# Optimization experiments

Hardware: AMD Instinct MI355X
Metric: run time of the kernel (lower is better)

## Reference

```python
import jax, jax.numpy as jnp
import numpy as np

B, N, E = 4, 2048, 512
H = 8
HD = E // H
HIDDEN = 3 * E  # split_ratio=3
EPS = 1e-5


def _layernorm(x, g, b):
    mu = jnp.mean(x, axis=-1, keepdims=True)
    var = jnp.var(x, axis=-1, keepdims=True)
    return (x - mu) * jax.lax.rsqrt(var + EPS) * g + b


def setup_inputs() -> dict:
    key = jax.random.key(0)
    ks = jax.random.split(key, 7)
    s = 0.02
    return {
        "x": jax.random.normal(ks[0], (B, N, E), jnp.float32),
        "qkv_w": jax.random.normal(ks[1], (E, 3 * E), jnp.float32) * s,
        "qkv_b": jax.random.normal(ks[2], (3 * E,), jnp.float32) * s,
        "fc1_w": jax.random.normal(ks[3], (E, HIDDEN), jnp.float32) * s,
        "fc1_b": jax.random.normal(ks[4], (HIDDEN,), jnp.float32) * s,
        "fc2_w": jax.random.normal(ks[5], (HIDDEN, E), jnp.float32) * s,
        "fc2_b": jax.random.normal(ks[6], (E,), jnp.float32) * s,
        "ln_att_g": jnp.ones((E,), jnp.float32),
        "ln_att_b": jnp.zeros((E,), jnp.float32),
        "ln_ffn_g": jnp.ones((E,), jnp.float32),
        "ln_ffn_b": jnp.zeros((E,), jnp.float32),
    }


def reference(x, qkv_w, qkv_b, fc1_w, fc1_b, fc2_w, fc2_b,
              ln_att_g, ln_att_b, ln_ffn_g, ln_ffn_b):
    # --- attention sub-block (pre-norm) ---
    h = x
    xn = _layernorm(x, ln_att_g, ln_att_b)
    qkv = xn @ qkv_w + qkv_b                     # [B,N,3E]
    qkv = qkv.reshape(B, N, H, 3 * HD).transpose(0, 2, 1, 3)  # [B,H,N,3*HD]
    q, k, v = jnp.split(qkv, 3, axis=-1)         # each [B,H,N,HD]
    scale = HD ** -0.5
    scores = jnp.einsum("bhnd,bhmd->bhnm", q, k) * scale
    attn = jax.nn.softmax(scores, axis=-1)
    out = jnp.einsum("bhnm,bhmd->bhnd", attn, v)
    out = out.transpose(0, 2, 1, 3).reshape(B, N, E)
    x = out + h
    # --- FFN sub-block (pre-norm) ---
    h = x
    xn = _layernorm(x, ln_ffn_g, ln_ffn_b)
    y = jax.nn.gelu(xn @ fc1_w + fc1_b, approximate=False)
    y = y @ fc2_w + fc2_b
    return y + h
```

## Files before the change

### kernel.cpp

```cpp
#include <hip/hip_runtime.h>
#include <hip/hip_bf16.h>
#include <math.h>

typedef unsigned short ushort_t;
typedef unsigned int   uint32;

typedef __bf16 bf16x8 __attribute__((ext_vector_type(8)));
typedef float  floatx4 __attribute__((ext_vector_type(4)));

__device__ __forceinline__ float lo16(uint32 u) { return __uint_as_float(u << 16); }
__device__ __forceinline__ float hi16(uint32 u) { return __uint_as_float(u & 0xFFFF0000u); }
__device__ __forceinline__ float b2f(ushort_t u) { return __uint_as_float(((uint32)u) << 16); }
__device__ __forceinline__ ushort_t f2b(float f) {
    uint32 x = __float_as_uint(f);
    x += 0x7FFFu + ((x >> 16) & 1u);
    return (ushort_t)(x >> 16);
}
__device__ __forceinline__ bool bf_mode(const uint32* sniff) {
    return *sniff == 0x3F803F80u;
}
__device__ __forceinline__ float rd(const void* p, size_t i, bool bf) {
    return bf ? b2f(((const ushort_t*)p)[i]) : ((const float*)p)[i];
}
__device__ __forceinline__ float4 rd4(const void* p, size_t i, bool bf) {
    if (bf) {
        uint2 u = *(const uint2*)((const ushort_t*)p + i);
        float4 r; r.x = lo16(u.x); r.y = hi16(u.x); r.z = lo16(u.y); r.w = hi16(u.y);
        return r;
    }
    return *(const float4*)((const float*)p + i);
}
__device__ __forceinline__ float fexp2(float x) {
#if __has_builtin(__builtin_amdgcn_exp2f)
    return __builtin_amdgcn_exp2f(x);
#else
    return exp2f(x);
#endif
}
__device__ __forceinline__ uint32 pack_bf16(float e0, float e1) {
#if __has_builtin(__builtin_amdgcn_perm)
    return __builtin_amdgcn_perm(__float_as_uint(e1), __float_as_uint(e0), 0x07060302u);
#else
    return (__float_as_uint(e0) >> 16) | (__float_as_uint(e1) & 0xFFFF0000u);
#endif
}
__device__ __forceinline__ void async_cp16(const ushort_t* g, ushort_t* l) {
    __builtin_amdgcn_global_load_lds(
        (const __attribute__((address_space(1))) void*)g,
        (__attribute__((address_space(3))) void*)l, 16, 0, 0);
}
__device__ __forceinline__ float gelu_f(float x) {
    float u = 0.79788456f * x * (1.0f + 0.044715f * x * x);
    u = fminf(u, 40.0f);
    float e = exp2f(u * 2.88539008f);
    return x * e * __builtin_amdgcn_rcpf(e + 1.0f);
}

__global__ __launch_bounds__(256)
void sentinel(float* out, float val, int n)
{
    int i = blockIdx.x * 256 + threadIdx.x;
    if (i < n) out[i] = val;
}

__global__ __launch_bounds__(256)
void conv_transpose3(const void* __restrict__ w0, const void* __restrict__ w1,
                     const void* __restrict__ w2, ushort_t* __restrict__ t0,
                     ushort_t* __restrict__ t1, ushort_t* __restrict__ t2,
                     const uint32* __restrict__ sniff)
{
    __shared__ ushort_t s[32][33];
    bool bf = bf_mode(sniff);
    int z = blockIdx.y;
    const void* W  = (z == 0) ? w0 : (z == 1) ? w1 : w2;
    ushort_t* Wt   = (z == 0) ? t0 : (z == 1) ? t1 : t2;
    int K = (z == 2) ? 1536 : 512;
    int N = (z == 2) ? 512 : 1536;
    int nb = N >> 5;
    int bx = blockIdx.x;
    int n0 = (bx % nb) * 32, k0 = (bx / nb) * 32;

    int tx = threadIdx.x & 31, ty = threadIdx.x >> 5;
#pragma unroll
    for (int i = 0; i < 4; i++) {
        int r = ty + i * 8;
        size_t idx = (size_t)(k0 + r) * N + (n0 + tx);
        s[r][tx] = f2b(rd(W, idx, bf));
    }
    __syncthreads();
#pragma unroll
    for (int i = 0; i < 4; i++) {
        int r = ty + i * 8;
        Wt[(size_t)(n0 + r) * K + (k0 + tx)] = s[tx][r];
    }
}

__global__ __launch_bounds__(256)
void v_transpose(const ushort_t* __restrict__ hbuf, ushort_t* __restrict__ vt)
{
    __shared__ ushort_t s[32][33];
    int tx = threadIdx.x & 31, ty = threadIdx.x >> 5;
    int n0 = blockIdx.x * 32, d0 = blockIdx.y * 32;
    int bh = blockIdx.z;
    int b = bh >> 3, h = bh & 7;
#pragma unroll
    for (int i = 0; i < 4; i++) {
        int r = ty + i * 8;
        s[r][tx] = hbuf[(size_t)(b * 2048 + n0 + r) * 1536 + h * 192 + 128 + d0 + tx];
    }
    __syncthreads();
#pragma unroll
    for (int i = 0; i < 4; i++) {
        int r = ty + i * 8;
        vt[((size_t)bh * 64 + d0 + r) * 2048 + n0 + tx] = s[tx][r];
    }
}

template <int XMODE>
__global__ __launch_bounds__(256)
void ln_any(const void* __restrict__ x, const void* __restrict__ g,
            const void* __restrict__ bta, ushort_t* __restrict__ out,
            const uint32* __restrict__ sniff)
{
    bool bf = bf_mode(sniff);
    int wid = threadIdx.x >> 6, lane = threadIdx.x & 63;
    int row = blockIdx.x * 4 + wid;
    size_t base = (size_t)row * 512 + (size_t)lane * 8;

    float4 v0, v1;
    if (XMODE == 2) { v0 = rd4(x, base, false); v1 = rd4(x, base + 4, false); }
    else            { v0 = rd4(x, base, bf);    v1 = rd4(x, base + 4, bf); }
    float v[8] = {v0.x, v0.y, v0.z, v0.w, v1.x, v1.y, v1.z, v1.w};

    float s = 0.f, ss = 0.f;
#pragma unroll
    for (int i = 0; i < 8; i++) { s += v[i]; ss += v[i] * v[i]; }
#pragma unroll
    for (int off = 32; off; off >>= 1) {
        s  += __shfl_xor(s, off);
        ss += __shfl_xor(ss, off);
    }
    float mu  = s * (1.0f / 512.0f);
    float var = ss * (1.0f / 512.0f) - mu * mu;
    float rs  = rsqrtf(var + 1e-5f);

    float4 g0 = rd4(g, lane * 8, bf), g1 = rd4(g, lane * 8 + 4, bf);
    float4 b0 = rd4(bta, lane * 8, bf), b1 = rd4(bta, lane * 8 + 4, bf);
    float gv[8] = {g0.x, g0.y, g0.z, g0.w, g1.x, g1.y, g1.z, g1.w};
    float bv[8] = {b0.x, b0.y, b0.z, b0.w, b1.x, b1.y, b1.z, b1.w};

    ushort_t o[8];
#pragma unroll
    for (int i = 0; i < 8; i++) o[i] = f2b((v[i] - mu) * rs * gv[i] + bv[i]);
    uint4 ov;
    ov.x = (uint32)o[0] | ((uint32)o[1] << 16);
    ov.y = (uint32)o[2] | ((uint32)o[3] << 16);
    ov.z = (uint32)o[4] | ((uint32)o[5] << 16);
    ov.w = (uint32)o[6] | ((uint32)o[7] << 16);
    *(uint4*)(out + base) = ov;
}

template <int TJ, int MODE>
__global__ __launch_bounds__(256)
void gemm_bt(const ushort_t* __restrict__ A, const ushort_t* __restrict__ Bt,
             const void* __restrict__ bias, void* C,
             const float* resid, int M, int N, int K,
             const uint32* __restrict__ sniff)
{
    constexpr int BN = 32 * TJ;
    __shared__ ushort_t As[128][32];
    __shared__ ushort_t Bs[BN][32];

    bool bf = bf_mode(sniff);
    int tid = threadIdx.x;
    int wid = tid >> 6, lane = tid & 63;

    int nwgx = gridDim.x;
    int wg   = blockIdx.y * nwgx + blockIdx.x;
    int cpx  = (nwgx * gridDim.y) >> 3;
    int swz  = (wg & 7) * cpx + (wg >> 3);
    int m0 = (swz / nwgx) * 128, n0 = (swz % nwgx) * BN;

    int wm = (wid >> 1) * 64, wn = (wid & 1) * (16 * TJ);
    int lm = lane & 15, kq = lane >> 4;

    floatx4 acc[4][TJ];
#pragma unroll
    for (int i = 0; i < 4; i++)
#pragma unroll
        for (int j = 0; j < TJ; j++) acc[i][j] = (floatx4)(0.f);

    for (int k0 = 0; k0 < K; k0 += 32) {
        __syncthreads();
#pragma unroll
        for (int i = 0; i < 2; i++) {
            int lin = i * 256 + tid;
            int r = lin >> 2, c8 = (lin & 3) * 8;
            async_cp16(&A[(size_t)(m0 + r) * K + k0 + c8], &As[r][c8]);
        }
#pragma unroll
        for (int i = 0; i < BN / 64; i++) {
            int lin = i * 256 + tid;
            int r = lin >> 2, c8 = (lin & 3) * 8;
            async_cp16(&Bt[(size_t)(n0 + r) * K + k0 + c8], &Bs[r][c8]);
        }
        __syncthreads();

        bf16x8 af[4], bfr[TJ];
#pragma unroll
        for (int ti = 0; ti < 4; ti++)
            af[ti] = *(const bf16x8*)&As[wm + ti * 16 + lm][kq * 8];
#pragma unroll
        for (int tj = 0; tj < TJ; tj++)
            bfr[tj] = *(const bf16x8*)&Bs[wn + tj * 16 + lm][kq * 8];
#pragma unroll
        for (int ti = 0; ti < 4; ti++)
#pragma unroll
            for (int tj = 0; tj < TJ; tj++)
                acc[ti][tj] = __builtin_amdgcn_mfma_f32_16x16x32_bf16(
                    af[ti], bfr[tj], acc[ti][tj], 0, 0, 0);
    }

    float bv[TJ];
#pragma unroll
    for (int tj = 0; tj < TJ; tj++) bv[tj] = rd(bias, n0 + wn + tj * 16 + lm, bf);
#pragma unroll
    for (int ti = 0; ti < 4; ti++) {
        int grow_base = m0 + wm + ti * 16 + kq * 4;
#pragma unroll
        for (int tj = 0; tj < TJ; tj++) {
            int gcol = n0 + wn + tj * 16 + lm;
#pragma unroll
            for (int r = 0; r < 4; r++) {
                int grow = grow_base + r;
                float v = acc[ti][tj][r] + bv[tj];
                if (MODE == 1) v = gelu_f(v);
                if (MODE == 2) {
                    float rv = resid[(size_t)grow * N + gcol];
                    ((float*)C)[(size_t)grow * N + gcol] = v + rv;
                } else {
                    ((ushort_t*)C)[(size_t)grow * N + gcol] = f2b(v);
                }
            }
        }
    }
}

template <int MODE>
__global__ __launch_bounds__(256)
void vgemm(const ushort_t* __restrict__ A, const void* __restrict__ W,
           const void* __restrict__ bias, void* C,
           const float* resid, int M, int N, int K,
             const uint32* __restrict__ sniff)
{
    __shared__ float Ast[32][33];
    __shared__ float Bs[32][36];

    bool bf = bf_mode(sniff);
    int t  = threadIdx.x;
    int tx = t & 15, ty = t >> 4;
    int m0 = blockIdx.y * 32, n0 = blockIdx.x * 32;
    int sr = t >> 3, sc4 = (t & 7) * 4;

    float a00 = 0.f, a01 = 0.f, a10 = 0.f, a11 = 0.f;

    for (int k0 = 0; k0 < K; k0 += 32) {
        __syncthreads();
        {
            uint2 u = *(const uint2*)&A[(size_t)(m0 + sr) * K + k0 + sc4];
            Ast[sc4 + 0][sr] = lo16(u.x);
            Ast[sc4 + 1][sr] = hi16(u.x);
            Ast[sc4 + 2][sr] = lo16(u.y);
            Ast[sc4 + 3][sr] = hi16(u.y);
        }
        {
            float4 w = rd4(W, (size_t)(k0 + sr) * N + n0 + sc4, bf);
            *(float4*)&Bs[sr][sc4] = w;
        }
        __syncthreads();

#pragma unroll
        for (int kk = 0; kk < 32; kk++) {
            float av0 = Ast[kk][ty], av1 = Ast[kk][ty + 16];
            float bv0 = Bs[kk][tx],  bv1 = Bs[kk][tx + 16];
            a00 += av0 * bv0; a01 += av0 * bv1;
            a10 += av1 * bv0; a11 += av1 * bv1;
        }
    }

    float accs[4] = {a00, a01, a10, a11};
#pragma unroll
    for (int q = 0; q < 4; q++) {
        int row = m0 + ty + (q >> 1) * 16;
        int col = n0 + tx + (q & 1) * 16;
        float v = accs[q] + rd(bias, col, bf);
        if (MODE == 1) v = gelu_f(v);
        if (MODE == 2) {
            float rv = resid[(size_t)row * N + col];
            ((float*)C)[(size_t)row * N + col] = v + rv;
        } else {
            ((ushort_t*)C)[(size_t)row * N + col] = f2b(v);
        }
    }
}

__global__ __launch_bounds__(256)
void attn_flash(const ushort_t* __restrict__ qkv, const ushort_t* __restrict__ vt,
                const void* __restrict__ x, float* __restrict__ out,
                const uint32* __restrict__ sniff)
{
    __shared__ ushort_t Kl[2][64][72];
    __shared__ ushort_t Vl[2][64][72];

    bool bf = bf_mode(sniff);
    int tid = threadIdx.x;
    int wid = tid >> 6, lane = tid & 63;
    int lm = lane & 15, quad = lane >> 4;

    int bid = blockIdx.x;
    int swz = (bid & 7) * 64 + (bid >> 3);
    int qt = swz & 15;
    int h  = (swz >> 4) & 7;
    int b  = swz >> 7;
    int bh = b * 8 + h;
    int q0 = qt * 128;

    const float SC = 0.18033688011f;

    bf16x8 qf[2][2];
#pragma unroll
    for (int g = 0; g < 2; g++) {
        const ushort_t* qp = qkv +
            ((size_t)(b * 2048 + q0 + wid * 32 + g * 16 + lm) * 1536 + h * 192);
        union { bf16x8 v; ushort_t u[8]; } qa0, qa1;
        qa0.v = *(const bf16x8*)(qp + quad * 8);
        qa1.v = *(const bf16x8*)(qp + 32 + quad * 8);
#pragma unroll
        for (int i = 0; i < 8; i++) {
            qa0.u[i] = f2b(b2f(qa0.u[i]) * SC);
            qa1.u[i] = f2b(b2f(qa1.u[i]) * SC);
        }
        qf[g][0] = qa0.v; qf[g][1] = qa1.v;
    }

    floatx4 oacc[2][4];
#pragma unroll
    for (int g = 0; g < 2; g++)
#pragma unroll
        for (int dt = 0; dt < 4; dt++) oacc[g][dt] = (floatx4)(0.f);
    float lsum[2] = {0.f, 0.f};

    int srow = tid >> 3;
    int sc8  = (tid & 7) * 8;

    const ushort_t* kb0 = qkv + ((size_t)(b * 2048 + srow)      * 1536 + h * 192 + 64 + sc8);
    const ushort_t* kb1 = qkv + ((size_t)(b * 2048 + 32 + srow) * 1536 + h * 192 + 64 + sc8);
    const ushort_t* vb0 = vt + ((size_t)bh * 64 + srow)      * 2048 + sc8;
    const ushort_t* vb1 = vt + ((size_t)bh * 64 + 32 + srow) * 2048 + sc8;

    uint4 kr0 = *(const uint4*)(kb0);
    uint4 kr1 = *(const uint4*)(kb1);
    uint4 vr0 = *(const uint4*)(vb0);
    uint4 vr1 = *(const uint4*)(vb1);
    *(uint4*)&Kl[0][srow][sc8]      = kr0;
    *(uint4*)&Kl[0][32 + srow][sc8] = kr1;
    *(uint4*)&Vl[0][srow][sc8]      = vr0;
    *(uint4*)&Vl[0][32 + srow][sc8] = vr1;
    kr0 = *(const uint4*)(kb0 + (size_t)64 * 1536);
    kr1 = *(const uint4*)(kb1 + (size_t)64 * 1536);
    vr0 = *(const uint4*)(vb0 + 64);
    vr1 = *(const uint4*)(vb1 + 64);
    __syncthreads();

    int addr0 = (lm + ((quad & 1) << 5)) << 2;
    int addr1 = addr0 + 64;
    bool hiq  = (quad >> 1) != 0;

    int p = 0;
    for (int kv = 0; kv < 2048; kv += 64) {
        if (kv < 2048 - 64) {
            *(uint4*)&Kl[p ^ 1][srow][sc8]      = kr0;
            *(uint4*)&Kl[p ^ 1][32 + srow][sc8] = kr1;
            *(uint4*)&Vl[p ^ 1][srow][sc8]      = vr0;
            *(uint4*)&Vl[p ^ 1][32 + srow][sc8] = vr1;
            int nkv = (kv + 128) & 2047;
            kr0 = *(const uint4*)(kb0 + (size_t)nkv * 1536);
            kr1 = *(const uint4*)(kb1 + (size_t)nkv * 1536);
            vr0 = *(const uint4*)(vb0 + nkv);
            vr1 = *(const uint4*)(vb1 + nkv);
        }

        floatx4 sacc[2][4];
#pragma unroll
        for (int g = 0; g < 2; g++)
#pragma unroll
            for (int t = 0; t < 4; t++) sacc[g][t] = (floatx4)(0.f);
        __builtin_amdgcn_s_setprio(1);
#pragma unroll
        for (int t = 0; t < 4; t++) {
            bf16x8 kf0 = *(const bf16x8*)&Kl[p][t * 16 + lm][quad * 8];
            bf16x8 kf1 = *(const bf16x8*)&Kl[p][t * 16 + lm][32 + quad * 8];
#pragma unroll
            for (int g = 0; g < 2; g++) {
                sacc[g][t] = __builtin_amdgcn_mfma_f32_16x16x32_bf16(kf0, qf[g][0], sacc[g][t], 0, 0, 0);
                sacc[g][t] = __builtin_amdgcn_mfma_f32_16x16x32_bf16(kf1, qf[g][1], sacc[g][t], 0, 0, 0);
            }
        }
        __builtin_amdgcn_s_setprio(0);

        uint32 pk[2][4][2];
#pragma unroll
        for (int g = 0; g < 2; g++) {
#pragma unroll
            for (int t = 0; t < 4; t++) {
                float e0 = fexp2(sacc[g][t][0]);
                float e1 = fexp2(sacc[g][t][1]);
                float e2 = fexp2(sacc[g][t][2]);
                float e3 = fexp2(sacc[g][t][3]);
                lsum[g] += (e0 + e1) + (e2 + e3);
                pk[g][t][0] = pack_bf16(e0, e1);
                pk[g][t][1] = pack_bf16(e2, e3);
            }
        }

        bf16x8 pf[2][2];
#pragma unroll
        for (int g = 0; g < 2; g++) {
#pragma unroll
            for (int c = 0; c < 2; c++) {
                uint32 pw[4];
#pragma unroll
                for (int j = 0; j < 4; j++) {
                    int ad = (j >> 1) ? addr1 : addr0;
                    int va = __builtin_amdgcn_ds_bpermute(ad, (int)pk[g][2 * c][j & 1]);
                    int vb = __builtin_amdgcn_ds_bpermute(ad, (int)pk[g][2 * c + 1][j & 1]);
                    pw[j] = (uint32)(hiq ? vb : va);
                }
                union { uint4 u; bf16x8 v; } cv;
                cv.u = make_uint4(pw[0], pw[1], pw[2], pw[3]);
                pf[g][c] = cv.v;
            }
        }

        __builtin_amdgcn_s_setprio(1);
#pragma unroll
        for (int dt = 0; dt < 4; dt++) {
            bf16x8 vf0 = *(const bf16x8*)&Vl[p][dt * 16 + lm][quad * 8];
            bf16x8 vf1 = *(const bf16x8*)&Vl[p][dt * 16 + lm][32 + quad * 8];
#pragma unroll
            for (int g = 0; g < 2; g++) {
                oacc[g][dt] = __builtin_amdgcn_mfma_f32_16x16x32_bf16(pf[g][0], vf0, oacc[g][dt], 0, 0, 0);
                oacc[g][dt] = __builtin_amdgcn_mfma_f32_16x16x32_bf16(pf[g][1], vf1, oacc[g][dt], 0, 0, 0);
            }
        }
        __builtin_amdgcn_s_setprio(0);

        __syncthreads();
        p ^= 1;
    }

    float rinv[2][4];
#pragma unroll
    for (int g = 0; g < 2; g++) {
        float rs = lsum[g];
        rs += __shfl_xor(rs, 16);
        rs += __shfl_xor(rs, 32);
        float ri = __builtin_amdgcn_rcpf(rs);
#pragma unroll
        for (int r = 0; r < 4; r++)
            rinv[g][r] = __shfl(ri, quad * 4 + r);
    }

#pragma unroll
    for (int g = 0; g < 2; g++)
#pragma unroll
        for (int dt = 0; dt < 4; dt++) {
#pragma unroll
            for (int r = 0; r < 4; r++) {
                int row = q0 + wid * 32 + g * 16 + quad * 4 + r;
                int col = h * 64 + dt * 16 + lm;
                size_t idx = (size_t)(b * 2048 + row) * 512 + col;
                out[idx] = oacc[g][dt][r] * rinv[g][r] + rd(x, idx, bf);
            }
        }
}

extern "C" void kernel_launch(void* const* d_in, const int* in_sizes, int n_in,
                              void* d_out, int out_size, void* d_ws, size_t ws_size,
                              hipStream_t stream)
{
    static const int expect[11] = {4194304, 786432, 1536, 786432, 1536, 786432,
                                   512, 512, 512, 512, 512};
    bool ok = (n_in == 11);
    if (ok) for (int i = 0; i < 11; i++) if (in_sizes[i] != expect[i]) { ok = false; break; }
    int nblk = (out_size + 255) / 256;
    if (!ok) {
        sentinel<<<nblk, 256, 0, stream>>>((float*)d_out, 1.0e6f, out_size);
        return;
    }
    if (ws_size < (size_t)33554432) {
        sentinel<<<nblk, 256, 0, stream>>>((float*)d_out, 2.0e6f, out_size);
        return;
    }

    const void* x     = d_in[0];
    const void* qkv_w = d_in[1];
    const void* qkv_b = d_in[2];
    const void* fc1_w = d_in[3];
    const void* fc1_b = d_in[4];
    const void* fc2_w = d_in[5];
    const void* fc2_b = d_in[6];
    const void* ln1g  = d_in[7];
    const void* ln1b  = d_in[8];
    const void* ln2g  = d_in[9];
    const void* ln2b  = d_in[10];
    const uint32* sniff = (const uint32*)d_in[7];

    char* ws = (char*)d_ws;
    ushort_t* xn   = (ushort_t*)(ws);
    ushort_t* hbuf = (ushort_t*)(ws + 8388608);
    float*    x2   = (float*)d_out;
    ushort_t* vt   = xn;

    bool mfma_path = (ws_size >= (size_t)38273024);

    if (mfma_path) {
        ushort_t* wtq = (ushort_t*)(ws + 33554432);
        ushort_t* wt1 = (ushort_t*)(ws + 35127296);
        ushort_t* wt2 = (ushort_t*)(ws + 36700160);

        conv_transpose3<<<dim3(768, 3), 256, 0, stream>>>(qkv_w, fc1_w, fc2_w,
                                                          wtq, wt1, wt2, sniff);
        ln_any<0><<<2048, 256, 0, stream>>>(x, ln1g, ln1b, xn, sniff);
        gemm_bt<4, 0><<<dim3(12, 64), 256, 0, stream>>>(xn, wtq, qkv_b, hbuf, nullptr,
                                                        8192, 1536, 512, sniff);
        v_transpose<<<dim3(64, 2, 32), 256, 0, stream>>>(hbuf, vt);
        attn_flash<<<512, 256, 0, stream>>>(hbuf, vt, x, x2, sniff);
        ln_any<2><<<2048, 256, 0, stream>>>(x2, ln2g, ln2b, xn, sniff);
        gemm_bt<4, 1><<<dim3(12, 64), 256, 0, stream>>>(xn, wt1, fc1_b, hbuf, nullptr,
                                                        8192, 1536, 512, sniff);
        gemm_bt<2, 2><<<dim3(8, 64), 256, 0, stream>>>(hbuf, wt2, fc2_b, d_out, x2,
                                                       8192, 512, 1536, sniff);
    } else {
        ln_any<0><<<2048, 256, 0, stream>>>(x, ln1g, ln1b, xn, sniff);
        vgemm<0><<<dim3(48, 256), 256, 0, stream>>>(xn, qkv_w, qkv_b, hbuf, nullptr,
                                                    8192, 1536, 512, sniff);
        v_transpose<<<dim3(64, 2, 32), 256, 0, stream>>>(hbuf, vt);
        attn_flash<<<512, 256, 0, stream>>>(hbuf, vt, x, x2, sniff);
        ln_any<2><<<2048, 256, 0, stream>>>(x2, ln2g, ln2b, xn, sniff);
        vgemm<1><<<dim3(48, 256), 256, 0, stream>>>(xn, fc1_w, fc1_b, hbuf, nullptr,
                                                    8192, 1536, 512, sniff);
        vgemm<2><<<dim3(16, 256), 256, 0, stream>>>(hbuf, fc2_w, fc2_b, d_out, x2,
                                                    8192, 512, 1536, sniff);
    }
}
```

Measured before the change: 260.6 us.

## Load K/V fragments directly from global into registers in single-wave attention blocks

The flash-attention kernel now runs one 64-thread wave per block, with 2048 blocks each covering 32 query rows. It drops the shared-memory K/V double buffer and its barriers. K fragments are software-pipelined in registers (prefetching the next tile while computing scores), and V fragments are loaded straight from global memory each iteration. This removes LDS traffic and __syncthreads, but K/V are no longer shared across four waves, so global/L2 read traffic rises about fourfold and latency is hidden only by register prefetch and occupancy.

```diff
diff --git a/kernel.cpp b/kernel.cpp
--- a/kernel.cpp
+++ b/kernel.cpp
@@ -304,26 +304,22 @@
     }
 }
 
-__global__ __launch_bounds__(256)
+__global__ __launch_bounds__(64)
 void attn_flash(const ushort_t* __restrict__ qkv, const ushort_t* __restrict__ vt,
                 const void* __restrict__ x, float* __restrict__ out,
                 const uint32* __restrict__ sniff)
 {
-    __shared__ ushort_t Kl[2][64][72];
-    __shared__ ushort_t Vl[2][64][72];
-
     bool bf = bf_mode(sniff);
-    int tid = threadIdx.x;
-    int wid = tid >> 6, lane = tid & 63;
+    int lane = threadIdx.x & 63;
     int lm = lane & 15, quad = lane >> 4;
 
     int bid = blockIdx.x;
-    int swz = (bid & 7) * 64 + (bid >> 3);
-    int qt = swz & 15;
-    int h  = (swz >> 4) & 7;
-    int b  = swz >> 7;
+    int swz = (bid & 7) * 256 + (bid >> 3);
+    int qt = swz & 63;
+    int h  = (swz >> 6) & 7;
+    int b  = swz >> 9;
     int bh = b * 8 + h;
-    int q0 = qt * 128;
+    int q0 = qt * 32;
 
     const float SC = 0.18033688011f;
 
@@ -331,7 +327,7 @@
 #pragma unroll
     for (int g = 0; g < 2; g++) {
         const ushort_t* qp = qkv +
-            ((size_t)(b * 2048 + q0 + wid * 32 + g * 16 + lm) * 1536 + h * 192);
+            ((size_t)(b * 2048 + q0 + g * 16 + lm) * 1536 + h * 192);
         union { bf16x8 v; ushort_t u[8]; } qa0, qa1;
         qa0.v = *(const bf16x8*)(qp + quad * 8);
         qa1.v = *(const bf16x8*)(qp + 32 + quad * 8);
@@ -350,45 +346,27 @@
         for (int dt = 0; dt < 4; dt++) oacc[g][dt] = (floatx4)(0.f);
     float lsum[2] = {0.f, 0.f};
 
-    int srow = tid >> 3;
-    int sc8  = (tid & 7) * 8;
-
-    const ushort_t* kb0 = qkv + ((size_t)(b * 2048 + srow)      * 1536 + h * 192 + 64 + sc8);
-    const ushort_t* kb1 = qkv + ((size_t)(b * 2048 + 32 + srow) * 1536 + h * 192 + 64 + sc8);
-    const ushort_t* vb0 = vt + ((size_t)bh * 64 + srow)      * 2048 + sc8;
-    const ushort_t* vb1 = vt + ((size_t)bh * 64 + 32 + srow) * 2048 + sc8;
-
-    uint4 kr0 = *(const uint4*)(kb0);
-    uint4 kr1 = *(const uint4*)(kb1);
-    uint4 vr0 = *(const uint4*)(vb0);
-    uint4 vr1 = *(const uint4*)(vb1);
-    *(uint4*)&Kl[0][srow][sc8]      = kr0;
-    *(uint4*)&Kl[0][32 + srow][sc8] = kr1;
-    *(uint4*)&Vl[0][srow][sc8]      = vr0;
-    *(uint4*)&Vl[0][32 + srow][sc8] = vr1;
-    kr0 = *(const uint4*)(kb0 + (size_t)64 * 1536);
-    kr1 = *(const uint4*)(kb1 + (size_t)64 * 1536);
-    vr0 = *(const uint4*)(vb0 + 64);
-    vr1 = *(const uint4*)(vb1 + 64);
-    __syncthreads();
+    const ushort_t* kfp = qkv + ((size_t)(b * 2048 + lm) * 1536 + h * 192 + 64 + quad * 8);
+    const ushort_t* vfp = vt + ((size_t)(bh * 64 + lm) * 2048 + quad * 8);
 
     int addr0 = (lm + ((quad & 1) << 5)) << 2;
     int addr1 = addr0 + 64;
     bool hiq  = (quad >> 1) != 0;
 
-    int p = 0;
-    for (int kv = 0; kv < 2048; kv += 64) {
-        if (kv < 2048 - 64) {
-            *(uint4*)&Kl[p ^ 1][srow][sc8]      = kr0;
-            *(uint4*)&Kl[p ^ 1][32 + srow][sc8] = kr1;
-            *(uint4*)&Vl[p ^ 1][srow][sc8]      = vr0;
-            *(uint4*)&Vl[p ^ 1][32 + srow][sc8] = vr1;
-            int nkv = (kv + 128) & 2047;
-            kr0 = *(const uint4*)(kb0 + (size_t)nkv * 1536);
-            kr1 = *(const uint4*)(kb1 + (size_t)nkv * 1536);
-            vr0 = *(const uint4*)(vb0 + nkv);
-            vr1 = *(const uint4*)(vb1 + nkv);
-        }
+    bf16x8 kfA[4][2], kfB[4][2];
+#pragma unroll
+    for (int t = 0; t < 4; t++)
+#pragma unroll
+        for (int c = 0; c < 2; c++)
+            kfA[t][c] = *(const bf16x8*)(kfp + (size_t)(t * 16) * 1536 + c * 32);
+
+    auto iter = [&](int kv, bf16x8 (&kfU)[4][2], bf16x8 (&kfP)[4][2], int nkv) {
+        bf16x8 vf[4][2];
+#pragma unroll
+        for (int dt = 0; dt < 4; dt++)
+#pragma unroll
+            for (int c = 0; c < 2; c++)
+                vf[dt][c] = *(const bf16x8*)(vfp + (size_t)(dt * 16) * 2048 + kv + c * 32);
 
         floatx4 sacc[2][4];
 #pragma unroll
@@ -398,15 +376,19 @@
         __builtin_amdgcn_s_setprio(1);
 #pragma unroll
         for (int t = 0; t < 4; t++) {
-            bf16x8 kf0 = *(const bf16x8*)&Kl[p][t * 16 + lm][quad * 8];
-            bf16x8 kf1 = *(const bf16x8*)&Kl[p][t * 16 + lm][32 + quad * 8];
 #pragma unroll
             for (int g = 0; g < 2; g++) {
-                sacc[g][t] = __builtin_amdgcn_mfma_f32_16x16x32_bf16(kf0, qf[g][0], sacc[g][t], 0, 0, 0);
-                sacc[g][t] = __builtin_amdgcn_mfma_f32_16x16x32_bf16(kf1, qf[g][1], sacc[g][t], 0, 0, 0);
+                sacc[g][t] = __builtin_amdgcn_mfma_f32_16x16x32_bf16(kfU[t][0], qf[g][0], sacc[g][t], 0, 0, 0);
+                sacc[g][t] = __builtin_amdgcn_mfma_f32_16x16x32_bf16(kfU[t][1], qf[g][1], sacc[g][t], 0, 0, 0);
             }
         }
         __builtin_amdgcn_s_setprio(0);
+
+#pragma unroll
+        for (int t = 0; t < 4; t++)
+#pragma unroll
+            for (int c = 0; c < 2; c++)
+                kfP[t][c] = *(const bf16x8*)(kfp + (size_t)(nkv + t * 16) * 1536 + c * 32);
 
         uint32 pk[2][4][2];
 #pragma unroll
@@ -445,18 +427,18 @@
         __builtin_amdgcn_s_setprio(1);
 #pragma unroll
         for (int dt = 0; dt < 4; dt++) {
-            bf16x8 vf0 = *(const bf16x8*)&Vl[p][dt * 16 + lm][quad * 8];
-            bf16x8 vf1 = *(const bf16x8*)&Vl[p][dt * 16 + lm][32 + quad * 8];
 #pragma unroll
             for (int g = 0; g < 2; g++) {
-                oacc[g][dt] = __builtin_amdgcn_mfma_f32_16x16x32_bf16(pf[g][0], vf0, oacc[g][dt], 0, 0, 0);
-                oacc[g][dt] = __builtin_amdgcn_mfma_f32_16x16x32_bf16(pf[g][1], vf1, oacc[g][dt], 0, 0, 0);
+                oacc[g][dt] = __builtin_amdgcn_mfma_f32_16x16x32_bf16(pf[g][0], vf[dt][0], oacc[g][dt], 0, 0, 0);
+                oacc[g][dt] = __builtin_amdgcn_mfma_f32_16x16x32_bf16(pf[g][1], vf[dt][1], oacc[g][dt], 0, 0, 0);
             }
         }
         __builtin_amdgcn_s_setprio(0);
-
-        __syncthreads();
-        p ^= 1;
+    };
+
+    for (int kv = 0; kv < 2048; kv += 128) {
+        iter(kv,      kfA, kfB, kv + 64);
+        iter(kv + 64, kfB, kfA, (kv + 128) & 2047);
     }
 
     float rinv[2][4];
@@ -477,7 +459,7 @@
         for (int dt = 0; dt < 4; dt++) {
 #pragma unroll
             for (int r = 0; r < 4; r++) {
-                int row = q0 + wid * 32 + g * 16 + quad * 4 + r;
+                int row = q0 + g * 16 + quad * 4 + r;
                 int col = h * 64 + dt * 16 + lm;
                 size_t idx = (size_t)(b * 2048 + row) * 512 + col;
                 out[idx] = oacc[g][dt][r] * rinv[g][r] + rd(x, idx, bf);
@@ -535,7 +517,7 @@
         gemm_bt<4, 0><<<dim3(12, 64), 256, 0, stream>>>(xn, wtq, qkv_b, hbuf, nullptr,
                                                         8192, 1536, 512, sniff);
         v_transpose<<<dim3(64, 2, 32), 256, 0, stream>>>(hbuf, vt);
-        attn_flash<<<512, 256, 0, stream>>>(hbuf, vt, x, x2, sniff);
+        attn_flash<<<2048, 64, 0, stream>>>(hbuf, vt, x, x2, sniff);
         ln_any<2><<<2048, 256, 0, stream>>>(x2, ln2g, ln2b, xn, sniff);
         gemm_bt<4, 1><<<dim3(12, 64), 256, 0, stream>>>(xn, wt1, fc1_b, hbuf, nullptr,
                                                         8192, 1536, 512, sniff);
@@ -546,7 +528,7 @@
         vgemm<0><<<dim3(48, 256), 256, 0, stream>>>(xn, qkv_w, qkv_b, hbuf, nullptr,
                                                     8192, 1536, 512, sniff);
         v_transpose<<<dim3(64, 2, 32), 256, 0, stream>>>(hbuf, vt);
-        attn_flash<<<512, 256, 0, stream>>>(hbuf, vt, x, x2, sniff);
+        attn_flash<<<2048, 64, 0, stream>>>(hbuf, vt, x, x2, sniff);
         ln_any<2><<<2048, 256, 0, stream>>>(x2, ln2g, ln2b, xn, sniff);
         vgemm<1><<<dim3(48, 256), 256, 0, stream>>>(xn, fc1_w, fc1_b, hbuf, nullptr,
                                                     8192, 1536, 512, sniff);
```

Measured after the change: 319.8 us. +22.7%, slower.

## Permute V transpose layout to drop bpermutes and split KV into two streams

Applied to the files above, without the earlier changes.

The V transpose kernel now writes columns in a permuted order. That lets the P fragments from the QK^T MFMA feed the PV MFMA directly, without the ds_bpermute shuffles. The attention loop also splits the 2048 keys into two halves processed together, with separate LDS double buffers and output accumulators that are summed at the end. This gives more independent MFMA work per iteration, at the cost of double the LDS, registers and global loads per step, which may reduce occupancy.

```diff
diff --git a/kernel.cpp b/kernel.cpp
--- a/kernel.cpp
+++ b/kernel.cpp
@@ -109,10 +109,11 @@
         s[r][tx] = hbuf[(size_t)(b * 2048 + n0 + r) * 1536 + h * 192 + 128 + d0 + tx];
     }
     __syncthreads();
+    int pt = ((tx & 12) << 1) | ((tx & 16) >> 2) | (tx & 3);
 #pragma unroll
     for (int i = 0; i < 4; i++) {
         int r = ty + i * 8;
-        vt[((size_t)bh * 64 + d0 + r) * 2048 + n0 + tx] = s[tx][r];
+        vt[((size_t)bh * 64 + d0 + r) * 2048 + n0 + pt] = s[tx][r];
     }
 }
 
@@ -309,8 +310,8 @@
                 const void* __restrict__ x, float* __restrict__ out,
                 const uint32* __restrict__ sniff)
 {
-    __shared__ ushort_t Kl[2][64][72];
-    __shared__ ushort_t Vl[2][64][72];
+    __shared__ ushort_t Kl[2][2][64][72];
+    __shared__ ushort_t Vl[2][2][64][72];
 
     bool bf = bf_mode(sniff);
     int tid = threadIdx.x;
@@ -343,114 +344,122 @@
         qf[g][0] = qa0.v; qf[g][1] = qa1.v;
     }
 
-    floatx4 oacc[2][4];
-#pragma unroll
-    for (int g = 0; g < 2; g++)
-#pragma unroll
-        for (int dt = 0; dt < 4; dt++) oacc[g][dt] = (floatx4)(0.f);
+    floatx4 oacc[2][2][4];
+#pragma unroll
+    for (int st = 0; st < 2; st++)
+#pragma unroll
+        for (int g = 0; g < 2; g++)
+#pragma unroll
+            for (int dt = 0; dt < 4; dt++) oacc[st][g][dt] = (floatx4)(0.f);
     float lsum[2] = {0.f, 0.f};
 
     int srow = tid >> 3;
     int sc8  = (tid & 7) * 8;
 
-    const ushort_t* kb0 = qkv + ((size_t)(b * 2048 + srow)      * 1536 + h * 192 + 64 + sc8);
-    const ushort_t* kb1 = qkv + ((size_t)(b * 2048 + 32 + srow) * 1536 + h * 192 + 64 + sc8);
-    const ushort_t* vb0 = vt + ((size_t)bh * 64 + srow)      * 2048 + sc8;
-    const ushort_t* vb1 = vt + ((size_t)bh * 64 + 32 + srow) * 2048 + sc8;
-
-    uint4 kr0 = *(const uint4*)(kb0);
-    uint4 kr1 = *(const uint4*)(kb1);
-    uint4 vr0 = *(const uint4*)(vb0);
-    uint4 vr1 = *(const uint4*)(vb1);
-    *(uint4*)&Kl[0][srow][sc8]      = kr0;
-    *(uint4*)&Kl[0][32 + srow][sc8] = kr1;
-    *(uint4*)&Vl[0][srow][sc8]      = vr0;
-    *(uint4*)&Vl[0][32 + srow][sc8] = vr1;
-    kr0 = *(const uint4*)(kb0 + (size_t)64 * 1536);
-    kr1 = *(const uint4*)(kb1 + (size_t)64 * 1536);
-    vr0 = *(const uint4*)(vb0 + 64);
-    vr1 = *(const uint4*)(vb1 + 64);
+    const ushort_t* kb[2];
+    const ushort_t* vb[2];
+#pragma unroll
+    for (int st = 0; st < 2; st++) {
+        kb[st] = qkv + ((size_t)(b * 2048 + st * 1024 + srow) * 1536 + h * 192 + 64 + sc8);
+        vb[st] = vt + ((size_t)(bh * 64 + srow) * 2048 + st * 1024 + sc8);
+    }
+
+    uint4 kr[2][2], vr[2][2];
+#pragma unroll
+    for (int st = 0; st < 2; st++) {
+        kr[st][0] = *(const uint4*)(kb[st]);
+        kr[st][1] = *(const uint4*)(kb[st] + (size_t)32 * 1536);
+        vr[st][0] = *(const uint4*)(vb[st]);
+        vr[st][1] = *(const uint4*)(vb[st] + (size_t)32 * 2048);
+        *(uint4*)&Kl[st][0][srow][sc8]      = kr[st][0];
+        *(uint4*)&Kl[st][0][32 + srow][sc8] = kr[st][1];
+        *(uint4*)&Vl[st][0][srow][sc8]      = vr[st][0];
+        *(uint4*)&Vl[st][0][32 + srow][sc8] = vr[st][1];
+        kr[st][0] = *(const uint4*)(kb[st] + (size_t)64 * 1536);
+        kr[st][1] = *(const uint4*)(kb[st] + (size_t)96 * 1536);
+        vr[st][0] = *(const uint4*)(vb[st] + 64);
+        vr[st][1] = *(const uint4*)(vb[st] + (size_t)32 * 2048 + 64);
+    }
     __syncthreads();
 
-    int addr0 = (lm + ((quad & 1) << 5)) << 2;
-    int addr1 = addr0 + 64;
-    bool hiq  = (quad >> 1) != 0;
-
     int p = 0;
-    for (int kv = 0; kv < 2048; kv += 64) {
-        if (kv < 2048 - 64) {
-            *(uint4*)&Kl[p ^ 1][srow][sc8]      = kr0;
-            *(uint4*)&Kl[p ^ 1][32 + srow][sc8] = kr1;
-            *(uint4*)&Vl[p ^ 1][srow][sc8]      = vr0;
-            *(uint4*)&Vl[p ^ 1][32 + srow][sc8] = vr1;
-            int nkv = (kv + 128) & 2047;
-            kr0 = *(const uint4*)(kb0 + (size_t)nkv * 1536);
-            kr1 = *(const uint4*)(kb1 + (size_t)nkv * 1536);
-            vr0 = *(const uint4*)(vb0 + nkv);
-            vr1 = *(const uint4*)(vb1 + nkv);
-        }
-
-        floatx4 sacc[2][4];
-#pragma unroll
-        for (int g = 0; g < 2; g++)
-#pragma unroll
-            for (int t = 0; t < 4; t++) sacc[g][t] = (floatx4)(0.f);
+    for (int kvl = 0; kvl < 1024; kvl += 64) {
+        if (kvl < 1024 - 64) {
+#pragma unroll
+            for (int st = 0; st < 2; st++) {
+                *(uint4*)&Kl[st][p ^ 1][srow][sc8]      = kr[st][0];
+                *(uint4*)&Kl[st][p ^ 1][32 + srow][sc8] = kr[st][1];
+                *(uint4*)&Vl[st][p ^ 1][srow][sc8]      = vr[st][0];
+                *(uint4*)&Vl[st][p ^ 1][32 + srow][sc8] = vr[st][1];
+            }
+            int nkv = (kvl + 128) & 1023;
+#pragma unroll
+            for (int st = 0; st < 2; st++) {
+                kr[st][0] = *(const uint4*)(kb[st] + (size_t)nkv * 1536);
+                kr[st][1] = *(const uint4*)(kb[st] + (size_t)(nkv + 32) * 1536);
+                vr[st][0] = *(const uint4*)(vb[st] + nkv);
+                vr[st][1] = *(const uint4*)(vb[st] + (size_t)32 * 2048 + nkv);
+            }
+        }
+
+        floatx4 sacc[2][2][4];
+#pragma unroll
+        for (int st = 0; st < 2; st++)
+#pragma unroll
+            for (int g = 0; g < 2; g++)
+#pragma unroll
+                for (int t = 0; t < 4; t++) sacc[st][g][t] = (floatx4)(0.f);
         __builtin_amdgcn_s_setprio(1);
 #pragma unroll
         for (int t = 0; t < 4; t++) {
-            bf16x8 kf0 = *(const bf16x8*)&Kl[p][t * 16 + lm][quad * 8];
-            bf16x8 kf1 = *(const bf16x8*)&Kl[p][t * 16 + lm][32 + quad * 8];
-#pragma unroll
-            for (int g = 0; g < 2; g++) {
-                sacc[g][t] = __builtin_amdgcn_mfma_f32_16x16x32_bf16(kf0, qf[g][0], sacc[g][t], 0, 0, 0);
-                sacc[g][t] = __builtin_amdgcn_mfma_f32_16x16x32_bf16(kf1, qf[g][1], sacc[g][t], 0, 0, 0);
+#pragma unroll
+            for (int st = 0; st < 2; st++) {
+                bf16x8 kf0 = *(const bf16x8*)&Kl[st][p][t * 16 + lm][quad * 8];
+                bf16x8 kf1 = *(const bf16x8*)&Kl[st][p][t * 16 + lm][32 + quad * 8];
+#pragma unroll
+                for (int g = 0; g < 2; g++) {
+                    sacc[st][g][t] = __builtin_amdgcn_mfma_f32_16x16x32_bf16(kf0, qf[g][0], sacc[st][g][t], 0, 0, 0);
+                    sacc[st][g][t] = __builtin_amdgcn_mfma_f32_16x16x32_bf16(kf1, qf[g][1], sacc[st][g][t], 0, 0, 0);
+                }
             }
         }
         __builtin_amdgcn_s_setprio(0);
 
-        uint32 pk[2][4][2];
-#pragma unroll
-        for (int g = 0; g < 2; g++) {
-#pragma unroll
-            for (int t = 0; t < 4; t++) {
-                float e0 = fexp2(sacc[g][t][0]);
-                float e1 = fexp2(sacc[g][t][1]);
-                float e2 = fexp2(sacc[g][t][2]);
-                float e3 = fexp2(sacc[g][t][3]);
-                lsum[g] += (e0 + e1) + (e2 + e3);
-                pk[g][t][0] = pack_bf16(e0, e1);
-                pk[g][t][1] = pack_bf16(e2, e3);
-            }
-        }
-
-        bf16x8 pf[2][2];
-#pragma unroll
-        for (int g = 0; g < 2; g++) {
-#pragma unroll
-            for (int c = 0; c < 2; c++) {
-                uint32 pw[4];
-#pragma unroll
-                for (int j = 0; j < 4; j++) {
-                    int ad = (j >> 1) ? addr1 : addr0;
-                    int va = __builtin_amdgcn_ds_bpermute(ad, (int)pk[g][2 * c][j & 1]);
-                    int vb = __builtin_amdgcn_ds_bpermute(ad, (int)pk[g][2 * c + 1][j & 1]);
-                    pw[j] = (uint32)(hiq ? vb : va);
+        uint32 pk[2][2][4][2];
+#pragma unroll
+        for (int st = 0; st < 2; st++)
+#pragma unroll
+            for (int g = 0; g < 2; g++)
+#pragma unroll
+                for (int t = 0; t < 4; t++) {
+                    float e0 = fexp2(sacc[st][g][t][0]);
+                    float e1 = fexp2(sacc[st][g][t][1]);
+                    float e2 = fexp2(sacc[st][g][t][2]);
+                    float e3 = fexp2(sacc[st][g][t][3]);
+                    lsum[st] = lsum[st];
+                    lsum[g]  += 0.f;
+                    pk[st][g][t][0] = pack_bf16(e0, e1);
+                    pk[st][g][t][1] = pack_bf16(e2, e3);
+                    lsum[g] += (e0 + e1) + (e2 + e3);
                 }
-                union { uint4 u; bf16x8 v; } cv;
-                cv.u = make_uint4(pw[0], pw[1], pw[2], pw[3]);
-                pf[g][c] = cv.v;
-            }
-        }
 
         __builtin_amdgcn_s_setprio(1);
 #pragma unroll
         for (int dt = 0; dt < 4; dt++) {
-            bf16x8 vf0 = *(const bf16x8*)&Vl[p][dt * 16 + lm][quad * 8];
-            bf16x8 vf1 = *(const bf16x8*)&Vl[p][dt * 16 + lm][32 + quad * 8];
-#pragma unroll
-            for (int g = 0; g < 2; g++) {
-                oacc[g][dt] = __builtin_amdgcn_mfma_f32_16x16x32_bf16(pf[g][0], vf0, oacc[g][dt], 0, 0, 0);
-                oacc[g][dt] = __builtin_amdgcn_mfma_f32_16x16x32_bf16(pf[g][1], vf1, oacc[g][dt], 0, 0, 0);
+#pragma unroll
+            for (int st = 0; st < 2; st++) {
+                bf16x8 vf0 = *(const bf16x8*)&Vl[st][p][dt * 16 + lm][quad * 8];
+                bf16x8 vf1 = *(const bf16x8*)&Vl[st][p][dt * 16 + lm][32 + quad * 8];
+#pragma unroll
+                for (int g = 0; g < 2; g++) {
+                    union { uint4 u; bf16x8 v; } c0, c1;
+                    c0.u = make_uint4(pk[st][g][0][0], pk[st][g][0][1],
+                                      pk[st][g][1][0], pk[st][g][1][1]);
+                    c1.u = make_uint4(pk[st][g][2][0], pk[st][g][2][1],
+                                      pk[st][g][3][0], pk[st][g][3][1]);
+                    oacc[st][g][dt] = __builtin_amdgcn_mfma_f32_16x16x32_bf16(c0.v, vf0, oacc[st][g][dt], 0, 0, 0);
+                    oacc[st][g][dt] = __builtin_amdgcn_mfma_f32_16x16x32_bf16(c1.v, vf1, oacc[st][g][dt], 0, 0, 0);
+                }
             }
         }
         __builtin_amdgcn_s_setprio(0);
@@ -458,6 +467,11 @@
         __syncthreads();
         p ^= 1;
     }
+
+#pragma unroll
+    for (int g = 0; g < 2; g++)
+#pragma unroll
+        for (int dt = 0; dt < 4; dt++) oacc[0][g][dt] += oacc[1][g][dt];
 
     float rinv[2][4];
 #pragma unroll
@@ -480,7 +494,7 @@
                 int row = q0 + wid * 32 + g * 16 + quad * 4 + r;
                 int col = h * 64 + dt * 16 + lm;
                 size_t idx = (size_t)(b * 2048 + row) * 512 + col;
-                out[idx] = oacc[g][dt][r] * rinv[g][r] + rd(x, idx, bf);
+                out[idx] = oacc[0][g][dt][r] * rinv[g][r] + rd(x, idx, bf);
             }
         }
 }
```

New measurement: 293.1 us. 1.12x slower.

## Split attention KV range across two warp groups and drop P-fragment bpermute shuffles

Applied to the files above, without the earlier changes.

The attention kernel now runs 512 threads per block, with two groups of four waves each handling half of the key/value sequence. The partial outputs and row sums are merged through shared memory at the end. Separately, the V transpose now writes columns in a permuted order so the exponentiated score registers can feed the PV MFMA directly, which removes the ds_bpermute register shuffles. This doubles the waves per query tile and cuts cross-lane traffic, at the cost of double the LDS buffers, an extra block-wide sync, and a final reduction step.

```diff
diff --git a/kernel.cpp b/kernel.cpp
--- a/kernel.cpp
+++ b/kernel.cpp
@@ -109,10 +109,11 @@
         s[r][tx] = hbuf[(size_t)(b * 2048 + n0 + r) * 1536 + h * 192 + 128 + d0 + tx];
     }
     __syncthreads();
+    int pt = ((tx & 12) << 1) | ((tx & 16) >> 2) | (tx & 3);
 #pragma unroll
     for (int i = 0; i < 4; i++) {
         int r = ty + i * 8;
-        vt[((size_t)bh * 64 + d0 + r) * 2048 + n0 + tx] = s[tx][r];
+        vt[((size_t)bh * 64 + d0 + r) * 2048 + n0 + pt] = s[tx][r];
     }
 }
 
@@ -304,17 +305,20 @@
     }
 }
 
-__global__ __launch_bounds__(256)
+__global__ __launch_bounds__(512)
 void attn_flash(const ushort_t* __restrict__ qkv, const ushort_t* __restrict__ vt,
                 const void* __restrict__ x, float* __restrict__ out,
                 const uint32* __restrict__ sniff)
 {
-    __shared__ ushort_t Kl[2][64][72];
-    __shared__ ushort_t Vl[2][64][72];
+    __shared__ ushort_t Kl[2][2][64][72];
+    __shared__ ushort_t Vl[2][2][64][72];
 
     bool bf = bf_mode(sniff);
     int tid = threadIdx.x;
-    int wid = tid >> 6, lane = tid & 63;
+    int wid = tid >> 6;
+    int wlocal = wid & 3;
+    int grp = wid >> 2;
+    int lane = tid & 63;
     int lm = lane & 15, quad = lane >> 4;
 
     int bid = blockIdx.x;
@@ -331,7 +335,7 @@
 #pragma unroll
     for (int g = 0; g < 2; g++) {
         const ushort_t* qp = qkv +
-            ((size_t)(b * 2048 + q0 + wid * 32 + g * 16 + lm) * 1536 + h * 192);
+            ((size_t)(b * 2048 + q0 + wlocal * 32 + g * 16 + lm) * 1536 + h * 192);
         union { bf16x8 v; ushort_t u[8]; } qa0, qa1;
         qa0.v = *(const bf16x8*)(qp + quad * 8);
         qa1.v = *(const bf16x8*)(qp + 32 + quad * 8);
@@ -350,40 +354,38 @@
         for (int dt = 0; dt < 4; dt++) oacc[g][dt] = (floatx4)(0.f);
     float lsum[2] = {0.f, 0.f};
 
-    int srow = tid >> 3;
-    int sc8  = (tid & 7) * 8;
-
-    const ushort_t* kb0 = qkv + ((size_t)(b * 2048 + srow)      * 1536 + h * 192 + 64 + sc8);
-    const ushort_t* kb1 = qkv + ((size_t)(b * 2048 + 32 + srow) * 1536 + h * 192 + 64 + sc8);
-    const ushort_t* vb0 = vt + ((size_t)bh * 64 + srow)      * 2048 + sc8;
-    const ushort_t* vb1 = vt + ((size_t)bh * 64 + 32 + srow) * 2048 + sc8;
+    int t256 = tid & 255;
+    int srow = t256 >> 3;
+    int sc8  = (t256 & 7) * 8;
+    int kv0  = grp * 1024;
+
+    const ushort_t* kb0 = qkv + ((size_t)(b * 2048 + kv0 + srow) * 1536 + h * 192 + 64 + sc8);
+    const ushort_t* kb1 = qkv + ((size_t)(b * 2048 + kv0 + 32 + srow) * 1536 + h * 192 + 64 + sc8);
+    const ushort_t* vb0 = vt + ((size_t)(bh * 64 + srow) * 2048 + kv0 + sc8);
+    const ushort_t* vb1 = vt + ((size_t)(bh * 64 + 32 + srow) * 2048 + kv0 + sc8);
 
     uint4 kr0 = *(const uint4*)(kb0);
     uint4 kr1 = *(const uint4*)(kb1);
     uint4 vr0 = *(const uint4*)(vb0);
     uint4 vr1 = *(const uint4*)(vb1);
-    *(uint4*)&Kl[0][srow][sc8]      = kr0;
-    *(uint4*)&Kl[0][32 + srow][sc8] = kr1;
-    *(uint4*)&Vl[0][srow][sc8]      = vr0;
-    *(uint4*)&Vl[0][32 + srow][sc8] = vr1;
+    *(uint4*)&Kl[grp][0][srow][sc8]      = kr0;
+    *(uint4*)&Kl[grp][0][32 + srow][sc8] = kr1;
+    *(uint4*)&Vl[grp][0][srow][sc8]      = vr0;
+    *(uint4*)&Vl[grp][0][32 + srow][sc8] = vr1;
     kr0 = *(const uint4*)(kb0 + (size_t)64 * 1536);
     kr1 = *(const uint4*)(kb1 + (size_t)64 * 1536);
     vr0 = *(const uint4*)(vb0 + 64);
     vr1 = *(const uint4*)(vb1 + 64);
     __syncthreads();
 
-    int addr0 = (lm + ((quad & 1) << 5)) << 2;
-    int addr1 = addr0 + 64;
-    bool hiq  = (quad >> 1) != 0;
-
     int p = 0;
-    for (int kv = 0; kv < 2048; kv += 64) {
-        if (kv < 2048 - 64) {
-            *(uint4*)&Kl[p ^ 1][srow][sc8]      = kr0;
-            *(uint4*)&Kl[p ^ 1][32 + srow][sc8] = kr1;
-            *(uint4*)&Vl[p ^ 1][srow][sc8]      = vr0;
-            *(uint4*)&Vl[p ^ 1][32 + srow][sc8] = vr1;
-            int nkv = (kv + 128) & 2047;
+    for (int kvl = 0; kvl < 1024; kvl += 64) {
+        if (kvl < 1024 - 64) {
+            *(uint4*)&Kl[grp][p ^ 1][srow][sc8]      = kr0;
+            *(uint4*)&Kl[grp][p ^ 1][32 + srow][sc8] = kr1;
+            *(uint4*)&Vl[grp][p ^ 1][srow][sc8]      = vr0;
+            *(uint4*)&Vl[grp][p ^ 1][32 + srow][sc8] = vr1;
+            int nkv = (kvl + 128) & 1023;
             kr0 = *(const uint4*)(kb0 + (size_t)nkv * 1536);
             kr1 = *(const uint4*)(kb1 + (size_t)nkv * 1536);
             vr0 = *(const uint4*)(vb0 + nkv);
@@ -398,8 +400,8 @@
         __builtin_amdgcn_s_setprio(1);
 #pragma unroll
         for (int t = 0; t < 4; t++) {
-            bf16x8 kf0 = *(const bf16x8*)&Kl[p][t * 16 + lm][quad * 8];
-            bf16x8 kf1 = *(const bf16x8*)&Kl[p][t * 16 + lm][32 + quad * 8];
+            bf16x8 kf0 = *(const bf16x8*)&Kl[grp][p][t * 16 + lm][quad * 8];
+            bf16x8 kf1 = *(const bf16x8*)&Kl[grp][p][t * 16 + lm][32 + quad * 8];
 #pragma unroll
             for (int g = 0; g < 2; g++) {
                 sacc[g][t] = __builtin_amdgcn_mfma_f32_16x16x32_bf16(kf0, qf[g][0], sacc[g][t], 0, 0, 0);
@@ -410,7 +412,7 @@
 
         uint32 pk[2][4][2];
 #pragma unroll
-        for (int g = 0; g < 2; g++) {
+        for (int g = 0; g < 2; g++)
 #pragma unroll
             for (int t = 0; t < 4; t++) {
                 float e0 = fexp2(sacc[g][t][0]);
@@ -421,36 +423,19 @@
                 pk[g][t][0] = pack_bf16(e0, e1);
                 pk[g][t][1] = pack_bf16(e2, e3);
             }
-        }
-
-        bf16x8 pf[2][2];
-#pragma unroll
-        for (int g = 0; g < 2; g++) {
-#pragma unroll
-            for (int c = 0; c < 2; c++) {
-                uint32 pw[4];
-#pragma unroll
-                for (int j = 0; j < 4; j++) {
-                    int ad = (j >> 1) ? addr1 : addr0;
-                    int va = __builtin_amdgcn_ds_bpermute(ad, (int)pk[g][2 * c][j & 1]);
-                    int vb = __builtin_amdgcn_ds_bpermute(ad, (int)pk[g][2 * c + 1][j & 1]);
-                    pw[j] = (uint32)(hiq ? vb : va);
-                }
-                union { uint4 u; bf16x8 v; } cv;
-                cv.u = make_uint4(pw[0], pw[1], pw[2], pw[3]);
-                pf[g][c] = cv.v;
-            }
-        }
 
         __builtin_amdgcn_s_setprio(1);
 #pragma unroll
         for (int dt = 0; dt < 4; dt++) {
-            bf16x8 vf0 = *(const bf16x8*)&Vl[p][dt * 16 + lm][quad * 8];
-            bf16x8 vf1 = *(const bf16x8*)&Vl[p][dt * 16 + lm][32 + quad * 8];
+            bf16x8 vf0 = *(const bf16x8*)&Vl[grp][p][dt * 16 + lm][quad * 8];
+            bf16x8 vf1 = *(const bf16x8*)&Vl[grp][p][dt * 16 + lm][32 + quad * 8];
 #pragma unroll
             for (int g = 0; g < 2; g++) {
-                oacc[g][dt] = __builtin_amdgcn_mfma_f32_16x16x32_bf16(pf[g][0], vf0, oacc[g][dt], 0, 0, 0);
-                oacc[g][dt] = __builtin_amdgcn_mfma_f32_16x16x32_bf16(pf[g][1], vf1, oacc[g][dt], 0, 0, 0);
+                union { uint4 u; bf16x8 v; } c0, c1;
+                c0.u = make_uint4(pk[g][0][0], pk[g][0][1], pk[g][1][0], pk[g][1][1]);
+                c1.u = make_uint4(pk[g][2][0], pk[g][2][1], pk[g][3][0], pk[g][3][1]);
+                oacc[g][dt] = __builtin_amdgcn_mfma_f32_16x16x32_bf16(c0.v, vf0, oacc[g][dt], 0, 0, 0);
+                oacc[g][dt] = __builtin_amdgcn_mfma_f32_16x16x32_bf16(c1.v, vf1, oacc[g][dt], 0, 0, 0);
             }
         }
         __builtin_amdgcn_s_setprio(0);
@@ -459,30 +444,54 @@
         p ^= 1;
     }
 
-    float rinv[2][4];
+    float lred[2];
 #pragma unroll
     for (int g = 0; g < 2; g++) {
         float rs = lsum[g];
         rs += __shfl_xor(rs, 16);
         rs += __shfl_xor(rs, 32);
-        float ri = __builtin_amdgcn_rcpf(rs);
-#pragma unroll
-        for (int r = 0; r < 4; r++)
-            rinv[g][r] = __shfl(ri, quad * 4 + r);
-    }
-
-#pragma unroll
-    for (int g = 0; g < 2; g++)
-#pragma unroll
-        for (int dt = 0; dt < 4; dt++) {
-#pragma unroll
-            for (int r = 0; r < 4; r++) {
-                int row = q0 + wid * 32 + g * 16 + quad * 4 + r;
-                int col = h * 64 + dt * 16 + lm;
-                size_t idx = (size_t)(b * 2048 + row) * 512 + col;
-                out[idx] = oacc[g][dt][r] * rinv[g][r] + rd(x, idx, bf);
-            }
-        }
+        lred[g] = rs;
+    }
+
+    float* Ofl = (float*)&Kl[0][0][0][0];
+    float* Lfl = Ofl + 128 * 68;
+    if (grp == 1) {
+#pragma unroll
+        for (int g = 0; g < 2; g++) {
+#pragma unroll
+            for (int dt = 0; dt < 4; dt++)
+#pragma unroll
+                for (int r = 0; r < 4; r++)
+                    Ofl[(wlocal * 32 + g * 16 + quad * 4 + r) * 68 + dt * 16 + lm]
+                        = oacc[g][dt][r];
+            if (quad == 0) Lfl[wlocal * 32 + g * 16 + lm] = lred[g];
+        }
+    }
+    __syncthreads();
+    if (grp == 0) {
+        float rinv[2][4];
+#pragma unroll
+        for (int g = 0; g < 2; g++) {
+            float rt = lred[g] + Lfl[wlocal * 32 + g * 16 + lm];
+            float ri = __builtin_amdgcn_rcpf(rt);
+#pragma unroll
+            for (int r = 0; r < 4; r++)
+                rinv[g][r] = __shfl(ri, quad * 4 + r);
+        }
+#pragma unroll
+        for (int g = 0; g < 2; g++)
+#pragma unroll
+            for (int dt = 0; dt < 4; dt++)
+#pragma unroll
+                for (int r = 0; r < 4; r++) {
+                    int rl = wlocal * 32 + g * 16 + quad * 4 + r;
+                    float o = oacc[g][dt][r] + Ofl[rl * 68 + dt * 16 + lm];
+                    int row = q0 + rl;
+                    int col = h * 64 + dt * 16 + lm;
+                    size_t idx = (size_t)(b * 2048 + row) * 512 + col;
+                    out[idx] = o * rinv[g][r] + rd(x, idx, bf);
+                }
+    }
 }
 
 extern "C" void kernel_launch(void* const* d_in, const int* in_sizes, int n_in,
@@ -535,7 +544,7 @@
         gemm_bt<4, 0><<<dim3(12, 64), 256, 0, stream>>>(xn, wtq, qkv_b, hbuf, nullptr,
                                                         8192, 1536, 512, sniff);
         v_transpose<<<dim3(64, 2, 32), 256, 0, stream>>>(hbuf, vt);
-        attn_flash<<<512, 256, 0, stream>>>(hbuf, vt, x, x2, sniff);
+        attn_flash<<<512, 512, 0, stream>>>(hbuf, vt, x, x2, sniff);
         ln_any<2><<<2048, 256, 0, stream>>>(x2, ln2g, ln2b, xn, sniff);
         gemm_bt<4, 1><<<dim3(12, 64), 256, 0, stream>>>(xn, wt1, fc1_b, hbuf, nullptr,
                                                         8192, 1536, 512, sniff);
@@ -546,7 +555,7 @@
         vgemm<0><<<dim3(48, 256), 256, 0, stream>>>(xn, qkv_w, qkv_b, hbuf, nullptr,
                                                     8192, 1536, 512, sniff);
         v_transpose<<<dim3(64, 2, 32), 256, 0, stream>>>(hbuf, vt);
-        attn_flash<<<512, 256, 0, stream>>>(hbuf, vt, x, x2, sniff);
+        attn_flash<<<512, 512, 0, stream>>>(hbuf, vt, x, x2, sniff);
         ln_any<2><<<2048, 256, 0, stream>>>(x2, ln2g, ln2b, xn, sniff);
         vgemm<1><<<dim3(48, 256), 256, 0, stream>>>(xn, fc1_w, fc1_b, hbuf, nullptr,
                                                     8192, 1536, 512, sniff);
```

Result: faster. 238.8 us (-8.4%).
